# Optimization experiments

Hardware: AMD Instinct MI355X
Metric: run time of the kernel (lower is better)

The kernel has to match this reference:

```python
import jax, jax.numpy as jnp
import numpy as np


def conv1x1(x, w, b):
    # x: [B,C,H,W], w: [O,C], b: [O]
    return jnp.einsum('bchw,oc->bohw', x, w) + b[None, :, None, None]


def resize_bilinear(x, h, w):
    # matches torch F.interpolate(mode='bilinear', align_corners=False), no antialias
    B, C = x.shape[:2]
    return jax.image.resize(x, (B, C, h, w), method='bilinear', antialias=False)


def attend(q_map, k_map, v_map, num_heads, scale):
    # q_map/k_map/v_map: [B, hidden, H, W] -> out [B, hidden, H, W]
    B, D, H, W = q_map.shape
    hd = D // num_heads
    N = H * W
    q = q_map.reshape(B, num_heads, hd, N).transpose(0, 1, 3, 2)  # [B,h,N,d]
    k = k_map.reshape(B, num_heads, hd, N)                         # [B,h,d,N]
    v = v_map.reshape(B, num_heads, hd, N).transpose(0, 1, 3, 2)  # [B,h,N,d]
    scores = jnp.einsum('bhnd,bhdm->bhnm', q, k) * scale
    attn = jax.nn.softmax(scores, axis=-1)
    out = jnp.einsum('bhnm,bhmd->bhnd', attn, v)                   # [B,h,N,d]
    return out.transpose(0, 1, 3, 2).reshape(B, D, H, W)


NUM_HEADS = 8
HIDDEN = 256
HEAD_DIM = HIDDEN // NUM_HEADS
SCALE = HEAD_DIM ** -0.5


def setup_inputs() -> dict:
    key = jax.random.key(0)
    ks = jax.random.split(key, 20)
    C_h, C_l = 128, 256
    inp = {
        'high_feat': jax.random.normal(ks[0], (2, C_h, 64, 64), jnp.float32),
        'low_feat': jax.random.normal(ks[1], (2, C_l, 32, 32), jnp.float32),
    }
    def lin(k, o, c):
        kw, kb = jax.random.split(k)
        s = 1.0 / np.sqrt(c)
        return (jax.random.uniform(kw, (o, c), jnp.float32, -s, s),
                jax.random.uniform(kb, (o,), jnp.float32, -s, s))
    inp['q_high_w'], inp['q_high_b'] = lin(ks[2], HIDDEN, C_h)
    inp['k_high_w'], inp['k_high_b'] = lin(ks[3], HIDDEN, C_h)
    inp['v_high_w'], inp['v_high_b'] = lin(ks[4], HIDDEN, C_h)
    inp['q_low_w'], inp['q_low_b'] = lin(ks[5], HIDDEN, C_l)
    inp['k_low_w'], inp['k_low_b'] = lin(ks[6], HIDDEN, C_l)
    inp['v_low_w'], inp['v_low_b'] = lin(ks[7], HIDDEN, C_l)
    inp['out_high_w'], inp['out_high_b'] = lin(ks[8], C_h, HIDDEN)
    inp['out_low_w'], inp['out_low_b'] = lin(ks[9], C_l, HIDDEN)
    return inp


def reference(high_feat, low_feat,
              q_high_w, q_high_b, k_high_w, k_high_b, v_high_w, v_high_b,
              q_low_w, q_low_b, k_low_w, k_low_b, v_low_w, v_low_b,
              out_high_w, out_high_b, out_low_w, out_low_b):
    B, C_h, H, W = high_feat.shape
    _, C_l, Hl, Wl = low_feat.shape

    # high queries attend to upsampled-low keys/values
    low_up = resize_bilinear(low_feat, H, W)
    q_h = conv1x1(high_feat, q_high_w, q_high_b)
    k_l = conv1x1(low_up, k_low_w, k_low_b)
    v_l = conv1x1(low_up, v_low_w, v_low_b)
    high_out = attend(q_h, k_l, v_l, NUM_HEADS, SCALE)
    high_out = conv1x1(high_out, out_high_w, out_high_b)

    # low queries attend to downsampled-high keys/values
    q_l = conv1x1(low_feat, q_low_w, q_low_b)
    k_h = resize_bilinear(conv1x1(high_feat, k_high_w, k_high_b), Hl, Wl)
    v_h = resize_bilinear(conv1x1(high_feat, v_high_w, v_high_b), Hl, Wl)
    low_out = attend(q_l, k_h, v_h, NUM_HEADS, SCALE)
    low_out = conv1x1(low_out, out_low_w, out_low_b)

    return (high_out, low_out)
```

## Files before the change

### kernel.cpp

```cpp
#include <hip/hip_runtime.h>
#include <hip/hip_bf16.h>

#define HEADS 8
#define HD    32

typedef __attribute__((ext_vector_type(8))) short short8;
typedef __attribute__((ext_vector_type(4))) float f32x4;
typedef unsigned short us;

__device__ __forceinline__ us f2bf(float f) {
  union { __hip_bfloat16 h; us u; } cv;
  cv.h = __float2bfloat16(f);
  return cv.u;
}
__device__ __forceinline__ float bf2f(us u) {
  union { float f; unsigned int i; } cv;
  cv.i = ((unsigned int)u) << 16;
  return cv.f;
}
__device__ __forceinline__ float exp2_native(float x) {
  float r;
  asm("v_exp_f32 %0, %1" : "=v"(r) : "v"(x));
  return r;
}
__device__ __forceinline__ void glds16(const us* g, us* l) {
  __builtin_amdgcn_global_load_lds(
      (const __attribute__((address_space(1))) void*)g,
      (__attribute__((address_space(3))) void*)l, 16, 0, 0);
}

struct GP {
  const void* X;
  const void* X2;
  const float* den;
  const float* W; const float* bias; void* out;
  int C, O, N, omode; float alpha;
};

template<int XMODE>
__global__ __launch_bounds__(256) void gemm_conv(
    GP g0, GP g1, GP g2, GP g3, int nb0, int nb1, int nb2) {
  __shared__ __align__(16) us Wh[2][64 * 32], Wl[2][64 * 32];
  __shared__ __align__(16) us Xh[2][64 * 32], Xl[2][64 * 32];
  int bid = blockIdx.x;
  GP g;
  if (bid < nb0) g = g0;
  else if (bid < nb0 + nb1) { g = g1; bid -= nb0; }
  else if (bid < nb0 + nb1 + nb2) { g = g2; bid -= nb0 + nb1; }
  else { g = g3; bid -= nb0 + nb1 + nb2; }
  const int C = g.C, O = g.O, N = g.N;
  int nx = N >> 6, nyo = O >> 6;
  int b = bid / (nx * nyo);
  int rr = bid - b * (nx * nyo);
  int o0 = (rr / nx) << 6;
  int n0 = (rr - (rr / nx) * nx) << 6;

  int tid = threadIdx.x, w = tid >> 6, l = tid & 63, lq = l & 15, l4 = l >> 4;

  int wr = tid >> 2, wcb = tid & 3;
  int xn = tid & 63, xcg = tid >> 6;
  const float* Wp = g.W + (size_t)(o0 + wr) * C + wcb * 8;
  const float* Xf = (const float*)g.X;
  const float* Xf2 = (const float*)g.X2;
  const unsigned int* Xp = (const unsigned int*)g.X;
  size_t xbase = (size_t)b * C * N + n0 + xn;
  int wof = wr * 32 + ((wcb ^ ((wr >> 1) & 3)) << 3);
  int xof = xn * 32 + ((xcg ^ ((xn >> 1) & 3)) << 3);

  auto stage = [&](int s, int bufi) {
    int c0 = s << 5;
    float4 wa = *(const float4*)(Wp + c0);
    float4 wb = *(const float4*)(Wp + c0 + 4);
    float wv[8] = {wa.x, wa.y, wa.z, wa.w, wb.x, wb.y, wb.z, wb.w};
    short8 whv, wlv;
#pragma unroll
    for (int j = 0; j < 8; ++j) {
      us h = f2bf(wv[j]);
      whv[j] = (short)h;
      wlv[j] = (short)f2bf(wv[j] - bf2f(h));
    }
    *(short8*)&Wh[bufi][wof] = whv;
    *(short8*)&Wl[bufi][wof] = wlv;
    float inv = 0.f;
    if constexpr (XMODE == 2) {
      size_t doff = ((size_t)(b * 8 + (c0 >> 5))) * N + n0 + xn;
      inv = 1.f / (g.den[doff] + g.den[(size_t)16 * N + doff]);
    }
    short8 xhv, xlv;
#pragma unroll
    for (int j = 0; j < 8; ++j) {
      int c = c0 + xcg * 8 + j;
      if constexpr (XMODE == 0) {
        float xv = Xf[xbase + (size_t)c * N];
        us h = f2bf(xv);
        xhv[j] = (short)h;
        xlv[j] = (short)f2bf(xv - bf2f(h));
      } else if constexpr (XMODE == 1) {
        unsigned int xv = Xp[xbase + (size_t)c * N];
        xhv[j] = (short)(xv >> 16);
        xlv[j] = (short)(xv & 0xffffu);
      } else {
        float xv = (Xf[xbase + (size_t)c * N] + Xf2[xbase + (size_t)c * N]) * inv;
        us h = f2bf(xv);
        xhv[j] = (short)h;
        xlv[j] = (short)f2bf(xv - bf2f(h));
      }
    }
    *(short8*)&Xh[bufi][xof] = xhv;
    *(short8*)&Xl[bufi][xof] = xlv;
  };

  f32x4 acc[4] = {{0,0,0,0},{0,0,0,0},{0,0,0,0},{0,0,0,0}};
  int ns = C >> 5, cur = 0;
  stage(0, 0);
  for (int s = 0; s < ns; ++s) {
    __syncthreads();
    if (s + 1 < ns) stage(s + 1, cur ^ 1);
    int swz = (l4 ^ ((lq >> 1) & 3)) << 3;
    int arow = w * 16 + lq;
    short8 ah = *(const short8*)&Wh[cur][arow * 32 + swz];
    short8 al = *(const short8*)&Wl[cur][arow * 32 + swz];
    __builtin_amdgcn_s_setprio(1);
#pragma unroll
    for (int nf = 0; nf < 4; ++nf) {
      int brow = nf * 16 + lq;
      short8 bh = *(const short8*)&Xh[cur][brow * 32 + swz];
      short8 bl = *(const short8*)&Xl[cur][brow * 32 + swz];
      acc[nf] = __builtin_amdgcn_mfma_f32_16x16x32_bf16(ah, bh, acc[nf], 0, 0, 0);
      acc[nf] = __builtin_amdgcn_mfma_f32_16x16x32_bf16(ah, bl, acc[nf], 0, 0, 0);
      acc[nf] = __builtin_amdgcn_mfma_f32_16x16x32_bf16(al, bh, acc[nf], 0, 0, 0);
    }
    __builtin_amdgcn_s_setprio(0);
    cur ^= 1;
  }

  float bv[4];
#pragma unroll
  for (int r = 0; r < 4; ++r) bv[r] = g.bias[o0 + w * 16 + l4 * 4 + r];
  if (g.omode == 0) {
    us* ob = (us*)g.out;
#pragma unroll
    for (int nf = 0; nf < 4; ++nf) {
      ushort4 pk;
      pk.x = f2bf((acc[nf][0] + bv[0]) * g.alpha);
      pk.y = f2bf((acc[nf][1] + bv[1]) * g.alpha);
      pk.z = f2bf((acc[nf][2] + bv[2]) * g.alpha);
      pk.w = f2bf((acc[nf][3] + bv[3]) * g.alpha);
      *(ushort4*)&ob[((size_t)b * N + n0 + nf * 16 + lq) * O + o0 + w * 16 + l4 * 4] = pk;
    }
  } else if (g.omode == 1) {
    us* ob = (us*)g.out;
#pragma unroll
    for (int nf = 0; nf < 4; ++nf)
#pragma unroll
      for (int r = 0; r < 4; ++r)
        ob[((size_t)(b * O + o0 + w * 16 + l4 * 4 + r)) * N + n0 + nf * 16 + lq] =
            f2bf(acc[nf][r] + bv[r]);
  } else {
    float* of = (float*)g.out;
#pragma unroll
    for (int nf = 0; nf < 4; ++nf)
#pragma unroll
      for (int r = 0; r < 4; ++r)
        of[((size_t)(b * O + o0 + w * 16 + l4 * 4 + r)) * N + n0 + nf * 16 + lq] =
            acc[nf][r] + bv[r];
  }
}

__global__ __launch_bounds__(256) void upsample_both(
    const us* __restrict__ inT, us* __restrict__ outT,
    const us* __restrict__ inC, us* __restrict__ outC, int nbT, int BC) {
  if ((int)blockIdx.x < nbT) {
    int rowg = blockIdx.x * 4 + (threadIdx.x >> 6);
    int ch = (threadIdx.x & 63) * 4;
    int b = rowg >> 12, n = rowg & 4095;
    int y = n >> 6, x = n & 63;
    float sy = y * 0.5f - 0.25f, sx = x * 0.5f - 0.25f;
    int y0 = (int)floorf(sy), x0 = (int)floorf(sx);
    float fy = sy - (float)y0, fx = sx - (float)x0;
    int y0c = max(y0, 0), y1c = min(y0 + 1, 31);
    int x0c = max(x0, 0), x1c = min(x0 + 1, 31);
    const us* ip = inT + (size_t)b * 1024 * 256 + ch;
    ushort4 v00 = *(const ushort4*)&ip[(size_t)(y0c * 32 + x0c) * 256];
    ushort4 v01 = *(const ushort4*)&ip[(size_t)(y0c * 32 + x1c) * 256];
    ushort4 v10 = *(const ushort4*)&ip[(size_t)(y1c * 32 + x0c) * 256];
    ushort4 v11 = *(const ushort4*)&ip[(size_t)(y1c * 32 + x1c) * 256];
    float w00 = (1.f - fy) * (1.f - fx), w01 = (1.f - fy) * fx;
    float w10 = fy * (1.f - fx), w11 = fy * fx;
    ushort4 o;
    o.x = f2bf(w00 * bf2f(v00.x) + w01 * bf2f(v01.x) + w10 * bf2f(v10.x) + w11 * bf2f(v11.x));
    o.y = f2bf(w00 * bf2f(v00.y) + w01 * bf2f(v01.y) + w10 * bf2f(v10.y) + w11 * bf2f(v11.y));
    o.z = f2bf(w00 * bf2f(v00.z) + w01 * bf2f(v01.z) + w10 * bf2f(v10.z) + w11 * bf2f(v11.z));
    o.w = f2bf(w00 * bf2f(v00.w) + w01 * bf2f(v01.w) + w10 * bf2f(v10.w) + w11 * bf2f(v11.w));
    *(ushort4*)&outT[((size_t)b * 4096 + n) * 256 + ch] = o;
  } else {
    int t = ((int)blockIdx.x - nbT) * 256 + threadIdx.x;
    if (t >= BC * 64) return;
    int y = t & 63, bc = t >> 6;
    float sy = y * 0.5f - 0.25f;
    int y0 = (int)floorf(sy);
    float fy = sy - (float)y0;
    int y0c = max(y0, 0), y1c = min(y0 + 1, 31);
    const us* r0 = inC + (size_t)bc * 1024 + y0c * 32;
    const us* r1 = inC + (size_t)bc * 1024 + y1c * 32;
    float m[32];
#pragma unroll
    for (int j = 0; j < 32; j += 8) {
      short8 a = *(const short8*)(r0 + j);
      short8 c = *(const short8*)(r1 + j);
#pragma unroll
      for (int e = 0; e < 8; ++e)
        m[j + e] = (1.f - fy) * bf2f((us)a[e]) + fy * bf2f((us)c[e]);
    }
    us* op = outC + (size_t)bc * 4096 + y * 64;
    short8 o8;
#pragma unroll
    for (int xo = 0; xo < 64; ++xo) {
      int k = xo >> 1;
      float v;
      if (xo & 1) v = (k < 31) ? 0.75f * m[k] + 0.25f * m[k + 1] : m[31];
      else        v = (k > 0) ? 0.25f * m[k - 1] + 0.75f * m[k] : m[0];
      o8[xo & 7] = (short)f2bf(v);
      if ((xo & 7) == 7) *(short8*)(op + (xo & ~7)) = o8;
    }
  }
}

__global__ __launch_bounds__(256) void downsample_pack_k(
    const float* __restrict__ in, unsigned int* __restrict__ opk, int BC) {
  int t = blockIdx.x * 256 + threadIdx.x;
  if (t >= BC * 1024) return;
  int x = t & 31, y = (t >> 5) & 31, bc = t >> 10;
  const float* ip = in + (size_t)bc * 4096 + (y * 2) * 64 + x * 2;
  float v = 0.25f * (ip[0] + ip[1] + ip[64] + ip[65]);
  us h = f2bf(v);
  opk[t] = ((unsigned int)h << 16) | f2bf(v - bf2f(h));
}

__global__ __launch_bounds__(256) void attn_mfma(
    const us* __restrict__ qT0, const us* __restrict__ kT0,
    const us* __restrict__ vC0, float* __restrict__ pn0, float* __restrict__ pd0,
    int N0, int nb0,
    const us* __restrict__ qT1, const us* __restrict__ kT1,
    const us* __restrict__ vC1, float* __restrict__ pn1, float* __restrict__ pd1,
    int N1) {
  __shared__ __align__(16) us Kt[2][64 * 32];
  __shared__ __align__(16) us Vt[2][32 * 64];
  __shared__ __align__(16) us Pt[8][16 * 64];

  int bid = blockIdx.x;
  const us *qT, *kT, *vC; float *pn, *pd; int N, bh, qb, sp;
  if (bid < nb0) {
    qT = qT0; kT = kT0; vC = vC0; pn = pn0; pd = pd0; N = N0;
    int xcd = bid & 7, slot = bid >> 3, nqb2 = (N0 >> 7) * 2;
    int qs = slot % nqb2;
    bh = ((slot / nqb2) << 3) | xcd;
    qb = qs >> 1; sp = qs & 1;
  } else {
    bid -= nb0;
    qT = qT1; kT = kT1; vC = vC1; pn = pn1; pd = pd1; N = N1;
    int xcd = bid & 7, slot = bid >> 3, nqb2 = (N1 >> 7) * 2;
    int qs = slot % nqb2;
    bh = ((slot / nqb2) << 3) | xcd;
    qb = qs >> 1; sp = qs & 1;
  }
  int b = bh >> 3, h = bh & 7;
  int SK = N >> 1;
  int tid = threadIdx.x;
  int w = tid >> 6, l = tid & 63;
  int lq = l & 15, l4 = l >> 4;

  short8 qfrag[2];
#pragma unroll
  for (int g = 0; g < 2; ++g) {
    const us* qp = qT + ((size_t)(b * N + qb * 128 + g * 64 + w * 16 + lq)) * 256 +
                   h * 32 + l4 * 8;
    qfrag[g] = *(const short8*)qp;
  }

  int rK = w * 16 + (l >> 2);
  const us* gK = kT + ((size_t)(b * N + sp * SK + rK)) * 256 + h * 32 +
                 (((l & 3) ^ ((rK >> 1) & 3)) << 3);
  int dV = w * 8 + (l >> 3);
  const us* gV = vC + ((size_t)(b * 256 + h * 32 + dV)) * N + sp * SK +
                 (((l & 7) ^ (dV & 7)) << 3);

  f32x4 acc0[2] = {{0,0,0,0},{0,0,0,0}};
  f32x4 acc1[2] = {{0,0,0,0},{0,0,0,0}};
  f32x4 acc2[2] = {{0,0,0,0},{0,0,0,0}};
  short8 ones;
#pragma unroll
  for (int j = 0; j < 8; ++j) ones[j] = (short)0x3F80;

  glds16(gK, &Kt[0][w * 512]);
  glds16(gV, &Vt[0][w * 512]);

  int nt = SK >> 6, cur = 0;
  for (int t = 0; t < nt; ++t) {
    __syncthreads();
    if (t + 1 < nt) {
      glds16(gK + (size_t)(t + 1) * 64 * 256, &Kt[cur ^ 1][w * 512]);
      glds16(gV + (t + 1) * 64, &Vt[cur ^ 1][w * 512]);
    }
    const us* Kb = Kt[cur];
    const us* Vb = Vt[cur];

#pragma unroll
    for (int kg = 0; kg < 4; ++kg) {
      int key = kg * 16 + lq;
      short8 a = *(const short8*)&Kb[key * 32 + ((l4 ^ ((key >> 1) & 3)) << 3)];
      f32x4 zero = {0.f, 0.f, 0.f, 0.f};
      int key0 = kg * 16 + l4 * 4;
      int pof = lq * 64 + (((key0 >> 3) ^ (lq & 7)) << 3) + (key0 & 7);
#pragma unroll
      for (int g = 0; g < 2; ++g) {
        __builtin_amdgcn_s_setprio(1);
        f32x4 s = __builtin_amdgcn_mfma_f32_16x16x32_bf16(a, qfrag[g], zero, 0, 0, 0);
        __builtin_amdgcn_s_setprio(0);
        float p0 = exp2_native(s[0]);
        float p1 = exp2_native(s[1]);
        float p2 = exp2_native(s[2]);
        float p3 = exp2_native(s[3]);
        unsigned int r01, r23;
        asm("v_cvt_pk_bf16_f32 %0, %1, %2" : "=v"(r01) : "v"(p0), "v"(p1));
        asm("v_cvt_pk_bf16_f32 %0, %1, %2" : "=v"(r23) : "v"(p2), "v"(p3));
        uint2 pk; pk.x = r01; pk.y = r23;
        *(uint2*)&Pt[w * 2 + g][pof] = pk;
      }
    }

#pragma unroll
    for (int kh = 0; kh < 2; ++kh) {
      int d0 = lq, d1 = 16 + lq;
      short8 vf0 = *(const short8*)&Vb[d0 * 64 + (((kh * 4 + l4) ^ (d0 & 7)) << 3)];
      short8 vf1 = *(const short8*)&Vb[d1 * 64 + (((kh * 4 + l4) ^ (d1 & 7)) << 3)];
      int pof = lq * 64 + (((kh * 4 + l4) ^ (lq & 7)) << 3);
#pragma unroll
      for (int g = 0; g < 2; ++g) {
        short8 pfr = *(const short8*)&Pt[w * 2 + g][pof];
        __builtin_amdgcn_s_setprio(1);
        acc0[g] = __builtin_amdgcn_mfma_f32_16x16x32_bf16(vf0, pfr, acc0[g], 0, 0, 0);
        acc1[g] = __builtin_amdgcn_mfma_f32_16x16x32_bf16(vf1, pfr, acc1[g], 0, 0, 0);
        acc2[g] = __builtin_amdgcn_mfma_f32_16x16x32_bf16(ones, pfr, acc2[g], 0, 0, 0);
        __builtin_amdgcn_s_setprio(0);
      }
    }
    cur ^= 1;
  }

  size_t nbase = ((size_t)((sp * 2 + b) * 8 + h)) * 32 * N;
  size_t dbase = ((size_t)((sp * 2 + b) * 8 + h)) * N;
#pragma unroll
  for (int g = 0; g < 2; ++g) {
    int q = qb * 128 + g * 64 + w * 16 + lq;
#pragma unroll
    for (int r = 0; r < 4; ++r) {
      pn[nbase + (size_t)(l4 * 4 + r) * N + q] = acc0[g][r];
      pn[nbase + (size_t)(16 + l4 * 4 + r) * N + q] = acc1[g][r];
    }
    if (l4 == 0) pd[dbase + q] = acc2[g][0];
  }
}

extern "C" void kernel_launch(void* const* d_in, const int* in_sizes, int n_in,
                              void* d_out, int out_size, void* d_ws, size_t ws_size,
                              hipStream_t stream) {
  const float* high_feat  = (const float*)d_in[0];
  const float* low_feat   = (const float*)d_in[1];
  const float* q_high_w   = (const float*)d_in[2];
  const float* q_high_b   = (const float*)d_in[3];
  const float* k_high_w   = (const float*)d_in[4];
  const float* k_high_b   = (const float*)d_in[5];
  const float* v_high_w   = (const float*)d_in[6];
  const float* v_high_b   = (const float*)d_in[7];
  const float* q_low_w    = (const float*)d_in[8];
  const float* q_low_b    = (const float*)d_in[9];
  const float* k_low_w    = (const float*)d_in[10];
  const float* k_low_b    = (const float*)d_in[11];
  const float* v_low_w    = (const float*)d_in[12];
  const float* v_low_b    = (const float*)d_in[13];
  const float* out_high_w = (const float*)d_in[14];
  const float* out_high_b = (const float*)d_in[15];
  const float* out_low_w  = (const float*)d_in[16];
  const float* out_low_b  = (const float*)d_in[17];

  const int B = 2, Nh = 4096, Nl = 1024;
  const float qa = 0.17677669529663689f * 1.4426950408889634f;

  char* p = (char*)d_ws;
  us* qT    = (us*)p; p += (size_t)2 * 4096 * 256 * 2;
  us* kTb   = (us*)p; p += (size_t)2 * 4096 * 256 * 2;
  us* vCb   = (us*)p; p += (size_t)2 * 256 * 4096 * 2;
  us* klbT  = (us*)p; p += (size_t)2 * 1024 * 256 * 2;
  us* vlb   = (us*)p; p += (size_t)2 * 256 * 1024 * 2;
  unsigned int* hfdn = (unsigned int*)p; p += (size_t)2 * 128 * 1024 * 4;
  us* qTl   = (us*)p; p += (size_t)2 * 1024 * 256 * 2;
  us* kTl   = (us*)p; p += (size_t)2 * 1024 * 256 * 2;
  us* vCl   = (us*)p; p += (size_t)2 * 256 * 1024 * 2;
  float* pnH = (float*)p; p += (size_t)2 * 16 * 32 * 4096 * 4;
  float* pdH = (float*)p; p += (size_t)2 * 16 * 4096 * 4;
  float* pnL = (float*)p; p += (size_t)2 * 16 * 32 * 1024 * 4;
  float* pdL = (float*)p; p += (size_t)2 * 16 * 1024 * 4;

  float* out_high = (float*)d_out;
  float* out_low  = out_high + 2 * 128 * 4096;

  downsample_pack_k<<<(B * 128 * 1024) / 256, 256, 0, stream>>>(high_feat, hfdn, B * 128);

  {
    GP s0 = {low_feat,  nullptr, nullptr, k_low_w,  k_low_b,  klbT, 256, 256, Nl, 0, 1.0f};
    GP s1 = {low_feat,  nullptr, nullptr, v_low_w,  v_low_b,  vlb,  256, 256, Nl, 1, 1.0f};
    GP s2 = {high_feat, nullptr, nullptr, q_high_w, q_high_b, qT,   128, 256, Nh, 0, qa};
    GP s3 = {low_feat,  nullptr, nullptr, q_low_w,  q_low_b,  qTl,  256, 256, Nl, 0, qa};
    gemm_conv<0><<<896, 256, 0, stream>>>(s0, s1, s2, s3, 128, 128, 512);
  }
  upsample_both<<<2048 + 128, 256, 0, stream>>>(klbT, kTb, vlb, vCb, 2048, B * 256);
  {
    GP s0 = {hfdn, nullptr, nullptr, k_high_w, k_high_b, kTl, 128, 256, Nl, 0, 1.0f};
    GP s1 = {hfdn, nullptr, nullptr, v_high_w, v_high_b, vCl, 128, 256, Nl, 1, 1.0f};
    gemm_conv<1><<<256, 256, 0, stream>>>(s0, s1, s0, s0, 128, 128, 0);
  }
  {
    int nb0 = 16 * (Nh / 128) * 2, nb1 = 16 * (Nl / 128) * 2;
    attn_mfma<<<nb0 + nb1, 256, 0, stream>>>(
        qT, kTb, vCb, pnH, pdH, Nh, nb0,
        qTl, kTl, vCl, pnL, pdL, Nl);
  }
  {
    GP s0 = {pnH, pnH + (size_t)512 * Nh, pdH, out_high_w, out_high_b, out_high,
             256, 128, Nh, 2, 1.0f};
    GP s1 = {pnL, pnL + (size_t)512 * Nl, pdL, out_low_w, out_low_b, out_low,
             256, 256, Nl, 2, 1.0f};
    gemm_conv<2><<<384, 256, 0, stream>>>(s0, s1, s0, s0, 256, 128, 0);
  }
}
```

Before: 110.0 us.

## Fuse downsample into projection GEMM, merge launches, and split high attention keys four ways

Removes the separate downsample-and-pack kernel by computing the 2x2 average inside the k/v-high projection GEMM. Those projections now run in the same launch as the other input projections, which drops two launches. The high-resolution attention now splits keys into 4 partitions instead of 2 to create more blocks, and the output GEMM sums a variable number of partial results. The trade-off is runtime branching on xmode in place of template specialisation, more partial-sum memory traffic, and redundant downsample reads in the GEMM.

```diff
diff --git a/kernel.cpp b/kernel.cpp
--- a/kernel.cpp
+++ b/kernel.cpp
@@ -31,15 +31,14 @@
 
 struct GP {
   const void* X;
-  const void* X2;
   const float* den;
   const float* W; const float* bias; void* out;
-  int C, O, N, omode; float alpha;
+  int C, O, N, omode, xmode, nsp; float alpha;
 };
 
-template<int XMODE>
 __global__ __launch_bounds__(256) void gemm_conv(
-    GP g0, GP g1, GP g2, GP g3, int nb0, int nb1, int nb2) {
+    GP g0, GP g1, GP g2, GP g3, GP g4, GP g5,
+    int nb0, int nb1, int nb2, int nb3, int nb4) {
   __shared__ __align__(16) us Wh[2][64 * 32], Wl[2][64 * 32];
   __shared__ __align__(16) us Xh[2][64 * 32], Xl[2][64 * 32];
   int bid = blockIdx.x;
@@ -47,7 +46,9 @@
   if (bid < nb0) g = g0;
   else if (bid < nb0 + nb1) { g = g1; bid -= nb0; }
   else if (bid < nb0 + nb1 + nb2) { g = g2; bid -= nb0 + nb1; }
-  else { g = g3; bid -= nb0 + nb1 + nb2; }
+  else if (bid < nb0 + nb1 + nb2 + nb3) { g = g3; bid -= nb0 + nb1 + nb2; }
+  else if (bid < nb0 + nb1 + nb2 + nb3 + nb4) { g = g4; bid -= nb0 + nb1 + nb2 + nb3; }
+  else { g = g5; bid -= nb0 + nb1 + nb2 + nb3 + nb4; }
   const int C = g.C, O = g.O, N = g.N;
   int nx = N >> 6, nyo = O >> 6;
   int b = bid / (nx * nyo);
@@ -61,8 +62,6 @@
   int xn = tid & 63, xcg = tid >> 6;
   const float* Wp = g.W + (size_t)(o0 + wr) * C + wcb * 8;
   const float* Xf = (const float*)g.X;
-  const float* Xf2 = (const float*)g.X2;
-  const unsigned int* Xp = (const unsigned int*)g.X;
   size_t xbase = (size_t)b * C * N + n0 + xn;
   int wof = wr * 32 + ((wcb ^ ((wr >> 1) & 3)) << 3);
   int xof = xn * 32 + ((xcg ^ ((xn >> 1) & 3)) << 3);
@@ -82,29 +81,32 @@
     *(short8*)&Wh[bufi][wof] = whv;
     *(short8*)&Wl[bufi][wof] = wlv;
     float inv = 0.f;
-    if constexpr (XMODE == 2) {
+    if (g.xmode == 2) {
       size_t doff = ((size_t)(b * 8 + (c0 >> 5))) * N + n0 + xn;
-      inv = 1.f / (g.den[doff] + g.den[(size_t)16 * N + doff]);
+      float dsum = 0.f;
+      for (int s2 = 0; s2 < g.nsp; ++s2) dsum += g.den[(size_t)s2 * 16 * N + doff];
+      inv = 1.f / dsum;
     }
     short8 xhv, xlv;
 #pragma unroll
     for (int j = 0; j < 8; ++j) {
       int c = c0 + xcg * 8 + j;
-      if constexpr (XMODE == 0) {
-        float xv = Xf[xbase + (size_t)c * N];
-        us h = f2bf(xv);
-        xhv[j] = (short)h;
-        xlv[j] = (short)f2bf(xv - bf2f(h));
-      } else if constexpr (XMODE == 1) {
-        unsigned int xv = Xp[xbase + (size_t)c * N];
-        xhv[j] = (short)(xv >> 16);
-        xlv[j] = (short)(xv & 0xffffu);
+      float xv;
+      if (g.xmode == 0) {
+        xv = Xf[xbase + (size_t)c * N];
+      } else if (g.xmode == 2) {
+        xv = 0.f;
+        for (int s2 = 0; s2 < g.nsp; ++s2)
+          xv += Xf[(size_t)s2 * 512 * N + xbase + (size_t)c * N];
+        xv *= inv;
       } else {
-        float xv = (Xf[xbase + (size_t)c * N] + Xf2[xbase + (size_t)c * N]) * inv;
-        us h = f2bf(xv);
-        xhv[j] = (short)h;
-        xlv[j] = (short)f2bf(xv - bf2f(h));
+        int n = n0 + xn, yy = n >> 5, xx = (n & 31) << 1;
+        const float* hp = Xf + ((size_t)(b * C + c)) * 4096 + yy * 128 + xx;
+        xv = 0.25f * (hp[0] + hp[1] + hp[64] + hp[65]);
       }
+      us h = f2bf(xv);
+      xhv[j] = (short)h;
+      xlv[j] = (short)f2bf(xv - bf2f(h));
     }
     *(short8*)&Xh[bufi][xof] = xhv;
     *(short8*)&Xl[bufi][xof] = xlv;
@@ -226,46 +228,32 @@
   }
 }
 
-__global__ __launch_bounds__(256) void downsample_pack_k(
-    const float* __restrict__ in, unsigned int* __restrict__ opk, int BC) {
-  int t = blockIdx.x * 256 + threadIdx.x;
-  if (t >= BC * 1024) return;
-  int x = t & 31, y = (t >> 5) & 31, bc = t >> 10;
-  const float* ip = in + (size_t)bc * 4096 + (y * 2) * 64 + x * 2;
-  float v = 0.25f * (ip[0] + ip[1] + ip[64] + ip[65]);
-  us h = f2bf(v);
-  opk[t] = ((unsigned int)h << 16) | f2bf(v - bf2f(h));
-}
-
 __global__ __launch_bounds__(256) void attn_mfma(
     const us* __restrict__ qT0, const us* __restrict__ kT0,
     const us* __restrict__ vC0, float* __restrict__ pn0, float* __restrict__ pd0,
-    int N0, int nb0,
+    int N0, int nb0, int nsp0,
     const us* __restrict__ qT1, const us* __restrict__ kT1,
     const us* __restrict__ vC1, float* __restrict__ pn1, float* __restrict__ pd1,
-    int N1) {
+    int N1, int nsp1) {
   __shared__ __align__(16) us Kt[2][64 * 32];
   __shared__ __align__(16) us Vt[2][32 * 64];
   __shared__ __align__(16) us Pt[8][16 * 64];
 
   int bid = blockIdx.x;
-  const us *qT, *kT, *vC; float *pn, *pd; int N, bh, qb, sp;
+  const us *qT, *kT, *vC; float *pn, *pd; int N, nsp;
   if (bid < nb0) {
-    qT = qT0; kT = kT0; vC = vC0; pn = pn0; pd = pd0; N = N0;
-    int xcd = bid & 7, slot = bid >> 3, nqb2 = (N0 >> 7) * 2;
-    int qs = slot % nqb2;
-    bh = ((slot / nqb2) << 3) | xcd;
-    qb = qs >> 1; sp = qs & 1;
+    qT = qT0; kT = kT0; vC = vC0; pn = pn0; pd = pd0; N = N0; nsp = nsp0;
   } else {
     bid -= nb0;
-    qT = qT1; kT = kT1; vC = vC1; pn = pn1; pd = pd1; N = N1;
-    int xcd = bid & 7, slot = bid >> 3, nqb2 = (N1 >> 7) * 2;
-    int qs = slot % nqb2;
-    bh = ((slot / nqb2) << 3) | xcd;
-    qb = qs >> 1; sp = qs & 1;
-  }
+    qT = qT1; kT = kT1; vC = vC1; pn = pn1; pd = pd1; N = N1; nsp = nsp1;
+  }
+  int xcd = bid & 7, slot = bid >> 3;
+  int nqb = N >> 7, per = nqb * nsp;
+  int qs = slot % per;
+  int bh = ((slot / per) << 3) | xcd;
+  int qb = qs / nsp, sp = qs % nsp;
   int b = bh >> 3, h = bh & 7;
-  int SK = N >> 1;
+  int SK = N / nsp;
   int tid = threadIdx.x;
   int w = tid >> 6, l = tid & 63;
   int lq = l & 15, l4 = l >> 4;
@@ -393,44 +381,38 @@
   us* vCb   = (us*)p; p += (size_t)2 * 256 * 4096 * 2;
   us* klbT  = (us*)p; p += (size_t)2 * 1024 * 256 * 2;
   us* vlb   = (us*)p; p += (size_t)2 * 256 * 1024 * 2;
-  unsigned int* hfdn = (unsigned int*)p; p += (size_t)2 * 128 * 1024 * 4;
   us* qTl   = (us*)p; p += (size_t)2 * 1024 * 256 * 2;
   us* kTl   = (us*)p; p += (size_t)2 * 1024 * 256 * 2;
   us* vCl   = (us*)p; p += (size_t)2 * 256 * 1024 * 2;
-  float* pnH = (float*)p; p += (size_t)2 * 16 * 32 * 4096 * 4;
-  float* pdH = (float*)p; p += (size_t)2 * 16 * 4096 * 4;
+  float* pnH = (float*)p; p += (size_t)4 * 16 * 32 * 4096 * 4;
+  float* pdH = (float*)p; p += (size_t)4 * 16 * 4096 * 4;
   float* pnL = (float*)p; p += (size_t)2 * 16 * 32 * 1024 * 4;
   float* pdL = (float*)p; p += (size_t)2 * 16 * 1024 * 4;
 
   float* out_high = (float*)d_out;
   float* out_low  = out_high + 2 * 128 * 4096;
 
-  downsample_pack_k<<<(B * 128 * 1024) / 256, 256, 0, stream>>>(high_feat, hfdn, B * 128);
+  GP z = {nullptr, nullptr, nullptr, nullptr, nullptr, 32, 64, 64, 2, 0, 1, 0.f};
 
   {
-    GP s0 = {low_feat,  nullptr, nullptr, k_low_w,  k_low_b,  klbT, 256, 256, Nl, 0, 1.0f};
-    GP s1 = {low_feat,  nullptr, nullptr, v_low_w,  v_low_b,  vlb,  256, 256, Nl, 1, 1.0f};
-    GP s2 = {high_feat, nullptr, nullptr, q_high_w, q_high_b, qT,   128, 256, Nh, 0, qa};
-    GP s3 = {low_feat,  nullptr, nullptr, q_low_w,  q_low_b,  qTl,  256, 256, Nl, 0, qa};
-    gemm_conv<0><<<896, 256, 0, stream>>>(s0, s1, s2, s3, 128, 128, 512);
+    GP s0 = {low_feat,  nullptr, k_low_w,  k_low_b,  klbT, 256, 256, Nl, 0, 0, 1, 1.0f};
+    GP s1 = {low_feat,  nullptr, v_low_w,  v_low_b,  vlb,  256, 256, Nl, 1, 0, 1, 1.0f};
+    GP s2 = {high_feat, nullptr, q_high_w, q_high_b, qT,   128, 256, Nh, 0, 0, 1, qa};
+    GP s3 = {low_feat,  nullptr, q_low_w,  q_low_b,  qTl,  256, 256, Nl, 0, 0, 1, qa};
+    GP s4 = {high_feat, nullptr, k_high_w, k_high_b, kTl,  128, 256, Nl, 0, 3, 1, 1.0f};
+    GP s5 = {high_feat, nullptr, v_high_w, v_high_b, vCl,  128, 256, Nl, 1, 3, 1, 1.0f};
+    gemm_conv<<<1152, 256, 0, stream>>>(s0, s1, s2, s3, s4, s5, 128, 128, 512, 128, 128);
   }
   upsample_both<<<2048 + 128, 256, 0, stream>>>(klbT, kTb, vlb, vCb, 2048, B * 256);
   {
-    GP s0 = {hfdn, nullptr, nullptr, k_high_w, k_high_b, kTl, 128, 256, Nl, 0, 1.0f};
-    GP s1 = {hfdn, nullptr, nullptr, v_high_w, v_high_b, vCl, 128, 256, Nl, 1, 1.0f};
-    gemm_conv<1><<<256, 256, 0, stream>>>(s0, s1, s0, s0, 128, 128, 0);
+    int nb0 = 16 * (Nh / 128) * 4, nb1 = 16 * (Nl / 128) * 2;
+    attn_mfma<<<nb0 + nb1, 256, 0, stream>>>(
+        qT, kTb, vCb, pnH, pdH, Nh, nb0, 4,
+        qTl, kTl, vCl, pnL, pdL, Nl, 2);
   }
   {
-    int nb0 = 16 * (Nh / 128) * 2, nb1 = 16 * (Nl / 128) * 2;
-    attn_mfma<<<nb0 + nb1, 256, 0, stream>>>(
-        qT, kTb, vCb, pnH, pdH, Nh, nb0,
-        qTl, kTl, vCl, pnL, pdL, Nl);
-  }
-  {
-    GP s0 = {pnH, pnH + (size_t)512 * Nh, pdH, out_high_w, out_high_b, out_high,
-             256, 128, Nh, 2, 1.0f};
-    GP s1 = {pnL, pnL + (size_t)512 * Nl, pdL, out_low_w, out_low_b, out_low,
-             256, 256, Nl, 2, 1.0f};
-    gemm_conv<2><<<384, 256, 0, stream>>>(s0, s1, s0, s0, 256, 128, 0);
-  }
-}
+    GP s0 = {pnH, pdH, out_high_w, out_high_b, out_high, 256, 128, Nh, 2, 2, 4, 1.0f};
+    GP s1 = {pnL, pdL, out_low_w,  out_low_b,  out_low,  256, 256, Nl, 2, 2, 2, 1.0f};
+    gemm_conv<<<384, 256, 0, stream>>>(s0, s1, z, z, z, z, 256, 128, 0, 0, 0);
+  }
+}
```

New measurement: 182.1 us. +65.5%, slower.
